# Kernel tuning notes

Hardware: AMD Instinct MI355X
Metric: run time of the kernel (lower is better)

Reference implementation:

```python
import jax, jax.numpy as jnp
import numpy as np

EPS = 1e-5  # BatchNorm eps


def setup_inputs() -> dict:
    key = jax.random.key(0)
    ks = jax.random.split(key, 13)
    B, C, H, W = 8, 256, 64, 64
    Ci = 128
    s = 0.05
    return {
        "x": jax.random.normal(ks[0], (B, C, H, W), jnp.float32),
        "Wt": jax.random.normal(ks[1], (Ci, C), jnp.float32) * s,
        "bt": jax.random.normal(ks[2], (Ci,), jnp.float32) * s,
        "Wp": jax.random.normal(ks[3], (Ci, C), jnp.float32) * s,
        "bp": jax.random.normal(ks[4], (Ci,), jnp.float32) * s,
        "Wg": jax.random.normal(ks[5], (Ci, C), jnp.float32) * s,
        "bg": jax.random.normal(ks[6], (Ci,), jnp.float32) * s,
        "Wz": jax.random.normal(ks[7], (C, Ci), jnp.float32) * s,
        "bz": jax.random.normal(ks[8], (C,), jnp.float32) * s,
        "gamma": jax.random.normal(ks[9], (C,), jnp.float32) * s,
        "beta": jax.random.normal(ks[10], (C,), jnp.float32) * s,
        "rmean": jax.random.normal(ks[11], (C,), jnp.float32) * s,
        "rvar": jax.random.uniform(ks[12], (C,), jnp.float32, 0.5, 1.5),
    }


def reference(x, Wt, bt, Wp, bp, Wg, bg, Wz, bz, gamma, beta, rmean, rvar):
    B, C, H, W = x.shape
    N = H * W
    xf = x.reshape(B, C, N)                                  # [B,C,N]
    # 1x1 conv projections == channel GEMMs
    theta = jnp.einsum('oc,bcn->bno', Wt, xf) + bt           # [B,N,Ci]
    phi = jnp.einsum('oc,bcn->bon', Wp, xf) + bp[:, None]    # [B,Ci,N]
    g = jnp.einsum('oc,bcn->bno', Wg, xf) + bg               # [B,N,Ci]
    # single-head attention over all N=H*W positions
    attn = jax.nn.softmax(jnp.einsum('bnc,bcm->bnm', theta, phi), axis=-1)
    y = jnp.einsum('bnm,bmc->bnc', attn, g)                  # [B,N,Ci]
    # W_z: 1x1 conv + BatchNorm (eval mode: running stats) + residual
    z = jnp.einsum('oc,bnc->bon', Wz, y) + bz[:, None]       # [B,C,N]
    inv = gamma / jnp.sqrt(rvar + EPS)                       # [C]
    zn = (z - rmean[:, None]) * inv[:, None] + beta[:, None]
    return zn.reshape(B, C, H, W) + x
```

## Files before the change

### kernel.cpp

```cpp
#include <hip/hip_runtime.h>
#include <stdint.h>

typedef __attribute__((ext_vector_type(8))) short bf16x8;
typedef __attribute__((ext_vector_type(4))) float f32x4;
typedef __attribute__((ext_vector_type(16))) float f32x16;

__device__ __forceinline__ unsigned short f32_to_bf16(float f) {
  union { float f; uint32_t u; } v; v.f = f;
  uint32_t u = v.u;
  u += 0x7fffu + ((u >> 16) & 1u);
  return (unsigned short)(u >> 16);
}

__device__ __forceinline__ float bf16_to_f32(unsigned short s) {
  union { uint32_t u; float f; } v; v.u = ((uint32_t)s) << 16;
  return v.f;
}

__device__ __forceinline__ uint32_t cvt_pk_bf16(float a, float b) {
  uint32_t r;
  asm("v_cvt_pk_bf16_f32 %0, %1, %2" : "=v"(r) : "v"(a), "v"(b));
  return r;
}

__device__ __forceinline__ void async_copy16(void* lds, const void* g) {
  __builtin_amdgcn_global_load_lds(
      (const __attribute__((address_space(1))) unsigned int*)g,
      (__attribute__((address_space(3))) unsigned int*)lds, 16, 0, 0);
}

__global__ __launch_bounds__(256) void wcvt_kernel(
    const float* __restrict__ Wt, const float* __restrict__ Wp,
    const float* __restrict__ Wg, const float* __restrict__ Wz,
    unsigned short* __restrict__ Wcat, unsigned short* __restrict__ Wzb) {
  int e = (blockIdx.x * 256 + threadIdx.x) * 4;
  const float* src;
  unsigned short* dst;
  int off;
  if (e < 32768) { src = Wt; dst = Wcat; off = e; }
  else if (e < 65536) { src = Wp; dst = Wcat + 32768; off = e - 32768; }
  else if (e < 98304) { src = Wg; dst = Wcat + 65536; off = e - 65536; }
  else { src = Wz; dst = Wzb; off = e - 98304; }
  float4 v = *(const float4*)(src + off);
  union { uint2 u; unsigned short s[4]; } pk;
  pk.s[0] = f32_to_bf16(v.x); pk.s[1] = f32_to_bf16(v.y);
  pk.s[2] = f32_to_bf16(v.z); pk.s[3] = f32_to_bf16(v.w);
  *(uint2*)(dst + off) = pk.u;
}

__global__ __launch_bounds__(512, 2) void proj_kernel(
    const float* __restrict__ x,
    const unsigned short* __restrict__ Wcat,
    const float* __restrict__ bt, const float* __restrict__ bp,
    const float* __restrict__ bg,
    unsigned short* __restrict__ Q, unsigned short* __restrict__ Km,
    unsigned short* __restrict__ Vt) {
  __shared__ __align__(1024) unsigned short xs[128 * 256];
  __shared__ unsigned short tmp[32][132];
  const int t = threadIdx.x;
  const int lane = t & 63;
  const int w = t >> 6;
  const int nt = blockIdx.x;
  const int b = blockIdx.y;
  const int n0 = nt * 128;

  const float* xb = x + (size_t)b * 256 * 4096;
  unsigned char* lbase = (unsigned char*)xs;

  for (int cc = 0; cc < 8; ++cc) {
#pragma unroll
    for (int i = 0; i < 2; ++i) {
      int idx = i * 512 + t;
      int c = idx >> 5;
      int n4 = (idx & 31) * 4;
      float4 v = *(const float4*)(xb + (size_t)(cc * 32 + c) * 4096 + n0 + n4);
      union { uint2 u; unsigned short s[4]; } pk;
      pk.s[0] = f32_to_bf16(v.x); pk.s[1] = f32_to_bf16(v.y);
      pk.s[2] = f32_to_bf16(v.z); pk.s[3] = f32_to_bf16(v.w);
      *(uint2*)&tmp[c][n4] = pk.u;
    }
    __syncthreads();
    {
      int n = t >> 2;
      int ch = t & 3;
      union { uint4 u; unsigned short s[8]; } pk;
#pragma unroll
      for (int jj = 0; jj < 8; ++jj) pk.s[jj] = tmp[ch * 8 + jj][n];
      int byt = n * 512 + ((cc * 64 + ch * 16) ^ ((n & 7) << 4));
      *(uint4*)(lbase + byt) = pk.u;
    }
    __syncthreads();
  }

  const int rl = lane & 15, gh = lane >> 4;
  const int swz = (rl & 7) << 4;
  const int rlv = (rl & 3) | ((rl & 4) << 1) | ((rl & 8) >> 1);

  f32x4 aQ[8], aK[8], aV[8];
#pragma unroll
  for (int i = 0; i < 8; ++i) {
    aQ[i] = (f32x4){0.f, 0.f, 0.f, 0.f};
    aK[i] = (f32x4){0.f, 0.f, 0.f, 0.f};
    aV[i] = (f32x4){0.f, 0.f, 0.f, 0.f};
  }

  const unsigned char* wq =
      (const unsigned char*)Wcat + ((w * 16 + rl) * 256) * 2 + gh * 16;
  const unsigned char* wk = wq + 128 * 512;
  const unsigned char* wv = wq + 256 * 512;

#pragma unroll
  for (int kk = 0; kk < 8; ++kk) {
    bf16x8 xf[8];
#pragma unroll
    for (int n2 = 0; n2 < 8; ++n2)
      xf[n2] = *(const bf16x8*)(lbase + (n2 * 16 + rl) * 512 +
                                ((kk * 64 + gh * 16) ^ swz));
    bf16x8 fq = *(const bf16x8*)(wq + kk * 64);
    bf16x8 fk = *(const bf16x8*)(wk + kk * 64);
    bf16x8 fv = *(const bf16x8*)(wv + kk * 64);
#pragma unroll
    for (int n2 = 0; n2 < 8; ++n2) {
      aQ[n2] = __builtin_amdgcn_mfma_f32_16x16x32_bf16(xf[n2], fq, aQ[n2], 0, 0, 0);
      aK[n2] = __builtin_amdgcn_mfma_f32_16x16x32_bf16(xf[n2], fk, aK[n2], 0, 0, 0);
      aV[n2] = __builtin_amdgcn_mfma_f32_16x16x32_bf16(fv, xf[n2], aV[n2], 0, 0, 0);
    }
  }

  const float btv = bt[w * 16 + rl];
  const float bpv = bp[w * 16 + rl];
  float bgv[4];
#pragma unroll
  for (int j = 0; j < 4; ++j) bgv[j] = bg[w * 16 + gh * 4 + j];

  unsigned short* Qb = Q + ((size_t)b * 4096 + n0) * 128 + w * 16 + rl;
  unsigned short* Kb = Km + ((size_t)b * 4096 + n0) * 128 + w * 16 + rl;
  unsigned short* Vb = Vt + (size_t)b * 128 * 4096 + n0 + rlv;
#pragma unroll
  for (int n2 = 0; n2 < 8; ++n2) {
#pragma unroll
    for (int j = 0; j < 4; ++j) {
      int n = n2 * 16 + gh * 4 + j;
      Qb[(size_t)n * 128] = f32_to_bf16(aQ[n2][j] + btv);
      Kb[(size_t)n * 128] = f32_to_bf16(aK[n2][j] + bpv);
      int o = w * 16 + gh * 4 + j;
      Vb[(size_t)o * 4096 + n2 * 16] = f32_to_bf16(aV[n2][j] + bgv[j]);
    }
  }
}

__global__ __launch_bounds__(256, 2) void attn_kernel(
    const unsigned short* __restrict__ Qg,
    const unsigned short* __restrict__ Kg,
    const unsigned short* __restrict__ Vg,
    unsigned short* __restrict__ Opart,
    float* __restrict__ Marr, float* __restrict__ Larr) {
  __shared__ __align__(1024) unsigned char smem[65536];
  const int t = threadIdx.x;
  const int lane = t & 63;
  const int w = t >> 6;
  const int q31 = lane & 31;
  const int hi = lane >> 5;
  const int kswz = (q31 & 15) << 4;

  const int orig = blockIdx.x;
  const int b = orig & 7;
  const int idx = orig >> 3;
  const int h = idx & 1;
  const int qg = idx >> 1;
  const int qw = qg * 128 + w * 32;
  const int kv0 = h * 2048;

  const unsigned short* Qb = Qg + (size_t)b * 4096 * 128;
  const unsigned short* Kb = Kg + (size_t)b * 4096 * 128;
  const unsigned short* Vb = Vg + (size_t)b * 128 * 4096;

  bf16x8 qf[8];
  {
    const unsigned char* qp =
        (const unsigned char*)(Qb + (size_t)(qw + q31) * 128) + hi * 16;
#pragma unroll
    for (int dc = 0; dc < 8; ++dc) qf[dc] = *(const bf16x8*)(qp + dc * 32);
  }

  const unsigned char* ksrc[4];
  const unsigned char* vsrc[4];
  unsigned int kofs[4], vofs[4];
#pragma unroll
  for (int ii = 0; ii < 4; ++ii) {
    int seg = w * 4 + ii;
    {
      int r = seg * 4 + (lane >> 4);
      int kcol = ((lane & 15) * 16) ^ ((r & 15) << 4);
      ksrc[ii] = (const unsigned char*)(Kb + (size_t)(kv0 + r) * 128) + kcol;
      kofs[ii] = seg * 1024;
    }
    {
      int o = seg * 1024 + lane * 16;
      int R = o >> 8;
      int cp = (o & 255) ^ ((R & 15) << 4);
      int d = 2 * R + (cp >> 7);
      int kvb = cp & 127;
      vsrc[ii] = (const unsigned char*)(Vb + (size_t)d * 4096 + kv0) + kvb;
      vofs[ii] = 16384 + seg * 1024;
    }
  }

  f32x16 acc[4];
#pragma unroll
  for (int i = 0; i < 4; ++i)
#pragma unroll
    for (int e = 0; e < 16; ++e) acc[i][e] = 0.f;
  float m = -1e30f, l = 0.f;

#pragma unroll
  for (int ii = 0; ii < 4; ++ii) {
    async_copy16(smem + kofs[ii], ksrc[ii]);
    async_copy16(smem + vofs[ii], vsrc[ii]);
  }
  __syncthreads();

#pragma unroll 2
  for (int it = 0; it < 32; ++it) {
    unsigned char* bb = smem + (it & 1) * 32768;
    if (it + 1 < 32) {
      unsigned int nb = ((it + 1) & 1) * 32768;
      size_t ko = (size_t)(it + 1) * 16384;
      int vo2 = (it + 1) * 128;
#pragma unroll
      for (int ii = 0; ii < 4; ++ii) {
        async_copy16(smem + nb + kofs[ii], ksrc[ii] + ko);
        async_copy16(smem + nb + vofs[ii], vsrc[ii] + vo2);
      }
    }

    f32x16 st0, st1;
#pragma unroll
    for (int e = 0; e < 16; ++e) { st0[e] = 0.f; st1[e] = 0.f; }
    const unsigned char* kb0 = bb + q31 * 256;
    const unsigned char* kb1 = bb + (32 + q31) * 256;
    __builtin_amdgcn_s_setprio(1);
#pragma unroll
    for (int dc = 0; dc < 8; ++dc) {
      int off = (dc * 32 + hi * 16) ^ kswz;
      bf16x8 k0 = *(const bf16x8*)(kb0 + off);
      bf16x8 k1 = *(const bf16x8*)(kb1 + off);
      st0 = __builtin_amdgcn_mfma_f32_32x32x16_bf16(k0, qf[dc], st0, 0, 0, 0);
      st1 = __builtin_amdgcn_mfma_f32_32x32x16_bf16(k1, qf[dc], st1, 0, 0, 0);
    }
    __builtin_amdgcn_s_setprio(0);

    float t8[8];
#pragma unroll
    for (int e = 0; e < 8; ++e)
      t8[e] = fmaxf(fmaxf(st0[e], st0[e + 8]), fmaxf(st1[e], st1[e + 8]));
#pragma unroll
    for (int e = 0; e < 4; ++e) t8[e] = fmaxf(t8[e], t8[e + 4]);
    float tl = fmaxf(fmaxf(t8[0], t8[1]), fmaxf(t8[2], t8[3]));
    if (__any(tl > m + 8.f)) {
      float tmax = tl;
#pragma unroll
      for (int off = 1; off < 64; off <<= 1)
        tmax = fmaxf(tmax, __shfl_xor(tmax, off));
      float mn = fmaxf(m, tmax);
      float sc = __expf(m - mn);
      m = mn;
      l *= sc;
#pragma unroll
      for (int i = 0; i < 4; ++i)
#pragma unroll
        for (int e = 0; e < 16; ++e) acc[i][e] *= sc;
    }
    float ls = 0.f;
#pragma unroll
    for (int e = 0; e < 16; ++e) { st0[e] = __expf(st0[e] - m); ls += st0[e]; }
#pragma unroll
    for (int e = 0; e < 16; ++e) { st1[e] = __expf(st1[e] - m); ls += st1[e]; }
    l += ls;

    const unsigned char* vbase = bb + 16384 + (q31 >> 1) * 256;
    const int vhb = (q31 & 1) << 7;
    const int vswz = (q31 >> 1) << 4;
#pragma unroll
    for (int ks = 0; ks < 4; ++ks) {
      union { uint32_t u[4]; bf16x8 v; } pk;
      if (ks == 0) {
        pk.u[0] = cvt_pk_bf16(st0[0], st0[1]);
        pk.u[1] = cvt_pk_bf16(st0[2], st0[3]);
        pk.u[2] = cvt_pk_bf16(st0[4], st0[5]);
        pk.u[3] = cvt_pk_bf16(st0[6], st0[7]);
      } else if (ks == 1) {
        pk.u[0] = cvt_pk_bf16(st0[8], st0[9]);
        pk.u[1] = cvt_pk_bf16(st0[10], st0[11]);
        pk.u[2] = cvt_pk_bf16(st0[12], st0[13]);
        pk.u[3] = cvt_pk_bf16(st0[14], st0[15]);
      } else if (ks == 2) {
        pk.u[0] = cvt_pk_bf16(st1[0], st1[1]);
        pk.u[1] = cvt_pk_bf16(st1[2], st1[3]);
        pk.u[2] = cvt_pk_bf16(st1[4], st1[5]);
        pk.u[3] = cvt_pk_bf16(st1[6], st1[7]);
      } else {
        pk.u[0] = cvt_pk_bf16(st1[8], st1[9]);
        pk.u[1] = cvt_pk_bf16(st1[10], st1[11]);
        pk.u[2] = cvt_pk_bf16(st1[12], st1[13]);
        pk.u[3] = cvt_pk_bf16(st1[14], st1[15]);
      }
      __builtin_amdgcn_s_setprio(1);
#pragma unroll
      for (int dt = 0; dt < 4; ++dt) {
        bf16x8 vf = *(const bf16x8*)(
            vbase + dt * 4096 + ((vhb | (ks * 32 + hi * 16)) ^ vswz));
        acc[dt] = __builtin_amdgcn_mfma_f32_32x32x16_bf16(pk.v, vf, acc[dt], 0, 0, 0);
      }
      __builtin_amdgcn_s_setprio(0);
    }
    __syncthreads();
  }

  float lf = l + __shfl_xor(l, 32);
  if (lane < 32) {
    size_t ix = (size_t)h * 32768 + (size_t)b * 4096 + qw + q31;
    Marr[ix] = m;
    Larr[ix] = lf;
  }
  unsigned short* ob = Opart + (size_t)h * 32768 * 128;
#pragma unroll
  for (int dt = 0; dt < 4; ++dt)
#pragma unroll
    for (int r = 0; r < 16; ++r) {
      int qrow = qw + (r & 3) + 8 * (r >> 2) + 4 * hi;
      ob[((size_t)b * 4096 + qrow) * 128 + dt * 32 + q31] =
          f32_to_bf16(acc[dt][r]);
    }
}

__global__ __launch_bounds__(512, 2) void outz_kernel(
    const unsigned short* __restrict__ Opart,
    const float* __restrict__ Marr, const float* __restrict__ Larr,
    const unsigned short* __restrict__ Wzb,
    const float* __restrict__ x, const float* __restrict__ bz,
    const float* __restrict__ gamma, const float* __restrict__ beta,
    const float* __restrict__ rmean, const float* __restrict__ rvar,
    float* __restrict__ out) {
  __shared__ __align__(1024) unsigned short ys[128 * 128];
  const int t = threadIdx.x;
  const int lane = t & 63;
  const int w = t >> 6;
  const int nt = blockIdx.x;
  const int b = blockIdx.y;
  const int n0 = nt * 128;

  unsigned char* lbase = (unsigned char*)ys;
#pragma unroll
  for (int i = 0; i < 4; ++i) {
    int off = (w * 4 + i) * 1024 + lane * 16;
    int n = off >> 8;
    int cb = (off & 255) ^ ((n & 7) << 4);
    size_t qidx = (size_t)b * 4096 + n0 + n;
    float m0 = Marr[qidx], m1 = Marr[32768 + qidx];
    float l0 = Larr[qidx], l1 = Larr[32768 + qidx];
    float M = fmaxf(m0, m1);
    float e0 = __expf(m0 - M), e1 = __expf(m1 - M);
    float rd = 1.f / (e0 * l0 + e1 * l1);
    float f0 = e0 * rd, f1 = e1 * rd;
    const unsigned char* ob = (const unsigned char*)Opart;
    const bf16x8 o0 = *(const bf16x8*)(ob + qidx * 256 + cb);
    const bf16x8 o1 = *(const bf16x8*)(ob + 32768ull * 256 + qidx * 256 + cb);
    union { uint4 u4; unsigned short s[8]; } pk;
#pragma unroll
    for (int e = 0; e < 8; ++e)
      pk.s[e] = f32_to_bf16(f0 * bf16_to_f32((unsigned short)o0[e]) +
                            f1 * bf16_to_f32((unsigned short)o1[e]));
    *(uint4*)(lbase + off) = pk.u4;
  }
  __syncthreads();

  const int rl = lane & 15, gh = lane >> 4;
  const int swz = (rl & 7) << 4;

  f32x4 acc[2][8];
#pragma unroll
  for (int i = 0; i < 2; ++i)
#pragma unroll
    for (int j = 0; j < 8; ++j) acc[i][j] = (f32x4){0.f, 0.f, 0.f, 0.f};

  const unsigned char* wz0 =
      (const unsigned char*)Wzb + ((w * 2) * 16 + rl) * 256 + gh * 16;

#pragma unroll
  for (int kk = 0; kk < 4; ++kk) {
    bf16x8 yf[8];
#pragma unroll
    for (int n2 = 0; n2 < 8; ++n2)
      yf[n2] = *(const bf16x8*)(lbase + (n2 * 16 + rl) * 256 +
                                ((kk * 64 + gh * 16) ^ swz));
    bf16x8 f0 = *(const bf16x8*)(wz0 + kk * 64);
    bf16x8 f1 = *(const bf16x8*)(wz0 + 16 * 256 + kk * 64);
#pragma unroll
    for (int n2 = 0; n2 < 8; ++n2) {
      acc[0][n2] = __builtin_amdgcn_mfma_f32_16x16x32_bf16(f0, yf[n2], acc[0][n2], 0, 0, 0);
      acc[1][n2] = __builtin_amdgcn_mfma_f32_16x16x32_bf16(f1, yf[n2], acc[1][n2], 0, 0, 0);
    }
  }

#pragma unroll
  for (int ot = 0; ot < 2; ++ot) {
#pragma unroll
    for (int j = 0; j < 4; ++j) {
      int o = (w * 2 + ot) * 16 + gh * 4 + j;
      float scale = gamma[o] * rsqrtf(rvar[o] + 1e-5f);
      float shift = (bz[o] - rmean[o]) * scale + beta[o];
      const float* xr = x + ((size_t)b * 256 + o) * 4096 + n0;
      float* orow = out + ((size_t)b * 256 + o) * 4096 + n0;
#pragma unroll
      for (int n2 = 0; n2 < 8; ++n2) {
        int n = n2 * 16 + rl;
        orow[n] = acc[ot][n2][j] * scale + shift + xr[n];
      }
    }
  }
}

extern "C" void kernel_launch(void* const* d_in, const int* in_sizes, int n_in,
                              void* d_out, int out_size, void* d_ws,
                              size_t ws_size, hipStream_t stream) {
  const float* x     = (const float*)d_in[0];
  const float* Wt    = (const float*)d_in[1];
  const float* bt    = (const float*)d_in[2];
  const float* Wp    = (const float*)d_in[3];
  const float* bp    = (const float*)d_in[4];
  const float* Wg    = (const float*)d_in[5];
  const float* bg    = (const float*)d_in[6];
  const float* Wz    = (const float*)d_in[7];
  const float* bz    = (const float*)d_in[8];
  const float* gamma = (const float*)d_in[9];
  const float* beta  = (const float*)d_in[10];
  const float* rmean = (const float*)d_in[11];
  const float* rvar  = (const float*)d_in[12];
  float* out = (float*)d_out;

  const size_t NE = (size_t)8 * 4096 * 128;
  unsigned short* Wcat  = (unsigned short*)d_ws;
  unsigned short* Wzb   = Wcat + 98304;
  float*          Marr  = (float*)(Wzb + 32768);
  float*          Larr  = Marr + 2 * 32768;
  unsigned short* Opart = (unsigned short*)(Larr + 2 * 32768);
  unsigned short* Q     = Opart + 2 * NE;
  unsigned short* Km    = Q + NE;
  unsigned short* Vt    = Km + NE;

  wcvt_kernel<<<128, 256, 0, stream>>>(Wt, Wp, Wg, Wz, Wcat, Wzb);
  proj_kernel<<<dim3(32, 8), 512, 0, stream>>>(x, Wcat, bt, bp, bg, Q, Km, Vt);
  attn_kernel<<<512, 256, 0, stream>>>(Q, Km, Vt, Opart, Marr, Larr);
  outz_kernel<<<dim3(32, 8), 512, 0, stream>>>(Opart, Marr, Larr, Wzb, x, bz,
                                               gamma, beta, rmean, rvar, out);
}
```

Baseline: 124.3 us.

## Process 64 query rows per wave in attention to reuse K/V fragments

Each attention wave now handles two 32-row query tiles that share every K and V fragment read from LDS. This halves LDS traffic per MFMA, and the block count drops from 512 to 256 since each block covers 256 queries. The cost is roughly double the accumulator and query registers, so launch bounds drop to one block per SM, unroll drops to 1, and only 256 blocks are launched, which leaves fewer waves to hide latency and may underfill the 256 CUs.

New measurement: 142.2 us. 14.4% more time.

```diff
diff --git a/kernel.cpp b/kernel.cpp
--- a/kernel.cpp
+++ b/kernel.cpp
@@ -149,7 +149,7 @@
   }
 }
 
-__global__ __launch_bounds__(256, 2) void attn_kernel(
+__global__ __launch_bounds__(256, 1) void attn_kernel(
     const unsigned short* __restrict__ Qg,
     const unsigned short* __restrict__ Kg,
     const unsigned short* __restrict__ Vg,
@@ -168,19 +168,23 @@
   const int idx = orig >> 3;
   const int h = idx & 1;
   const int qg = idx >> 1;
-  const int qw = qg * 128 + w * 32;
+  const int qw = qg * 256 + w * 64;
   const int kv0 = h * 2048;
 
   const unsigned short* Qb = Qg + (size_t)b * 4096 * 128;
   const unsigned short* Kb = Kg + (size_t)b * 4096 * 128;
   const unsigned short* Vb = Vg + (size_t)b * 128 * 4096;
 
-  bf16x8 qf[8];
+  bf16x8 qfA[8], qfB[8];
   {
-    const unsigned char* qp =
+    const unsigned char* qpA =
         (const unsigned char*)(Qb + (size_t)(qw + q31) * 128) + hi * 16;
-#pragma unroll
-    for (int dc = 0; dc < 8; ++dc) qf[dc] = *(const bf16x8*)(qp + dc * 32);
+    const unsigned char* qpB = qpA + 32 * 256;
+#pragma unroll
+    for (int dc = 0; dc < 8; ++dc) {
+      qfA[dc] = *(const bf16x8*)(qpA + dc * 32);
+      qfB[dc] = *(const bf16x8*)(qpB + dc * 32);
+    }
   }
 
   const unsigned char* ksrc[4];
@@ -206,12 +210,12 @@
     }
   }
 
-  f32x16 acc[4];
+  f32x16 accA[4], accB[4];
 #pragma unroll
   for (int i = 0; i < 4; ++i)
 #pragma unroll
-    for (int e = 0; e < 16; ++e) acc[i][e] = 0.f;
-  float m = -1e30f, l = 0.f;
+    for (int e = 0; e < 16; ++e) { accA[i][e] = 0.f; accB[i][e] = 0.f; }
+  float m = -1e30f, lA = 0.f, lB = 0.f;
 
 #pragma unroll
   for (int ii = 0; ii < 4; ++ii) {
@@ -220,7 +224,7 @@
   }
   __syncthreads();
 
-#pragma unroll 2
+#pragma unroll 1
   for (int it = 0; it < 32; ++it) {
     unsigned char* bb = smem + (it & 1) * 32768;
     if (it + 1 < 32) {
@@ -234,103 +238,97 @@
       }
     }
 
-    f32x16 st0, st1;
-#pragma unroll
-    for (int e = 0; e < 16; ++e) { st0[e] = 0.f; st1[e] = 0.f; }
-    const unsigned char* kb0 = bb + q31 * 256;
-    const unsigned char* kb1 = bb + (32 + q31) * 256;
-    __builtin_amdgcn_s_setprio(1);
-#pragma unroll
-    for (int dc = 0; dc < 8; ++dc) {
-      int off = (dc * 32 + hi * 16) ^ kswz;
-      bf16x8 k0 = *(const bf16x8*)(kb0 + off);
-      bf16x8 k1 = *(const bf16x8*)(kb1 + off);
-      st0 = __builtin_amdgcn_mfma_f32_32x32x16_bf16(k0, qf[dc], st0, 0, 0, 0);
-      st1 = __builtin_amdgcn_mfma_f32_32x32x16_bf16(k1, qf[dc], st1, 0, 0, 0);
-    }
-    __builtin_amdgcn_s_setprio(0);
-
-    float t8[8];
-#pragma unroll
-    for (int e = 0; e < 8; ++e)
-      t8[e] = fmaxf(fmaxf(st0[e], st0[e + 8]), fmaxf(st1[e], st1[e + 8]));
-#pragma unroll
-    for (int e = 0; e < 4; ++e) t8[e] = fmaxf(t8[e], t8[e + 4]);
-    float tl = fmaxf(fmaxf(t8[0], t8[1]), fmaxf(t8[2], t8[3]));
-    if (__any(tl > m + 8.f)) {
-      float tmax = tl;
-#pragma unroll
-      for (int off = 1; off < 64; off <<= 1)
-        tmax = fmaxf(tmax, __shfl_xor(tmax, off));
-      float mn = fmaxf(m, tmax);
-      float sc = __expf(m - mn);
-      m = mn;
-      l *= sc;
-#pragma unroll
-      for (int i = 0; i < 4; ++i)
-#pragma unroll
-        for (int e = 0; e < 16; ++e) acc[i][e] *= sc;
-    }
-    float ls = 0.f;
-#pragma unroll
-    for (int e = 0; e < 16; ++e) { st0[e] = __expf(st0[e] - m); ls += st0[e]; }
-#pragma unroll
-    for (int e = 0; e < 16; ++e) { st1[e] = __expf(st1[e] - m); ls += st1[e]; }
-    l += ls;
-
     const unsigned char* vbase = bb + 16384 + (q31 >> 1) * 256;
     const int vhb = (q31 & 1) << 7;
     const int vswz = (q31 >> 1) << 4;
-#pragma unroll
-    for (int ks = 0; ks < 4; ++ks) {
-      union { uint32_t u[4]; bf16x8 v; } pk;
-      if (ks == 0) {
-        pk.u[0] = cvt_pk_bf16(st0[0], st0[1]);
-        pk.u[1] = cvt_pk_bf16(st0[2], st0[3]);
-        pk.u[2] = cvt_pk_bf16(st0[4], st0[5]);
-        pk.u[3] = cvt_pk_bf16(st0[6], st0[7]);
-      } else if (ks == 1) {
-        pk.u[0] = cvt_pk_bf16(st0[8], st0[9]);
-        pk.u[1] = cvt_pk_bf16(st0[10], st0[11]);
-        pk.u[2] = cvt_pk_bf16(st0[12], st0[13]);
-        pk.u[3] = cvt_pk_bf16(st0[14], st0[15]);
-      } else if (ks == 2) {
-        pk.u[0] = cvt_pk_bf16(st1[0], st1[1]);
-        pk.u[1] = cvt_pk_bf16(st1[2], st1[3]);
-        pk.u[2] = cvt_pk_bf16(st1[4], st1[5]);
-        pk.u[3] = cvt_pk_bf16(st1[6], st1[7]);
-      } else {
-        pk.u[0] = cvt_pk_bf16(st1[8], st1[9]);
-        pk.u[1] = cvt_pk_bf16(st1[10], st1[11]);
-        pk.u[2] = cvt_pk_bf16(st1[12], st1[13]);
-        pk.u[3] = cvt_pk_bf16(st1[14], st1[15]);
-      }
+
+#pragma unroll
+    for (int tile = 0; tile < 2; ++tile) {
+      f32x16 sA, sB;
+#pragma unroll
+      for (int e = 0; e < 16; ++e) { sA[e] = 0.f; sB[e] = 0.f; }
+      const unsigned char* kb = bb + (tile * 32 + q31) * 256;
       __builtin_amdgcn_s_setprio(1);
 #pragma unroll
-      for (int dt = 0; dt < 4; ++dt) {
-        bf16x8 vf = *(const bf16x8*)(
-            vbase + dt * 4096 + ((vhb | (ks * 32 + hi * 16)) ^ vswz));
-        acc[dt] = __builtin_amdgcn_mfma_f32_32x32x16_bf16(pk.v, vf, acc[dt], 0, 0, 0);
+      for (int dc = 0; dc < 8; ++dc) {
+        bf16x8 kf = *(const bf16x8*)(kb + ((dc * 32 + hi * 16) ^ kswz));
+        sA = __builtin_amdgcn_mfma_f32_32x32x16_bf16(kf, qfA[dc], sA, 0, 0, 0);
+        sB = __builtin_amdgcn_mfma_f32_32x32x16_bf16(kf, qfB[dc], sB, 0, 0, 0);
       }
       __builtin_amdgcn_s_setprio(0);
+
+      float t8[8];
+#pragma unroll
+      for (int e = 0; e < 8; ++e)
+        t8[e] = fmaxf(fmaxf(sA[e], sA[e + 8]), fmaxf(sB[e], sB[e + 8]));
+#pragma unroll
+      for (int e = 0; e < 4; ++e) t8[e] = fmaxf(t8[e], t8[e + 4]);
+      float tl = fmaxf(fmaxf(t8[0], t8[1]), fmaxf(t8[2], t8[3]));
+      if (__any(tl > m + 8.f)) {
+        float tmax = tl;
+#pragma unroll
+        for (int off = 1; off < 64; off <<= 1)
+          tmax = fmaxf(tmax, __shfl_xor(tmax, off));
+        float mn = fmaxf(m, tmax);
+        float sc = __expf(m - mn);
+        m = mn;
+        lA *= sc; lB *= sc;
+#pragma unroll
+        for (int i = 0; i < 4; ++i)
+#pragma unroll
+          for (int e = 0; e < 16; ++e) { accA[i][e] *= sc; accB[i][e] *= sc; }
+      }
+      float a0 = 0.f, a1 = 0.f, b0 = 0.f, b1 = 0.f;
+#pragma unroll
+      for (int e = 0; e < 8; ++e) {
+        sA[e] = __expf(sA[e] - m);       a0 += sA[e];
+        sA[e + 8] = __expf(sA[e + 8] - m); a1 += sA[e + 8];
+        sB[e] = __expf(sB[e] - m);       b0 += sB[e];
+        sB[e + 8] = __expf(sB[e + 8] - m); b1 += sB[e + 8];
+      }
+      lA += a0 + a1;
+      lB += b0 + b1;
+
+#pragma unroll
+      for (int ksi = 0; ksi < 2; ++ksi) {
+        int ks = tile * 2 + ksi;
+        union { uint32_t u[4]; bf16x8 v; } pkA, pkB;
+#pragma unroll
+        for (int j = 0; j < 4; ++j) {
+          pkA.u[j] = cvt_pk_bf16(sA[ksi * 8 + j * 2], sA[ksi * 8 + j * 2 + 1]);
+          pkB.u[j] = cvt_pk_bf16(sB[ksi * 8 + j * 2], sB[ksi * 8 + j * 2 + 1]);
+        }
+        __builtin_amdgcn_s_setprio(1);
+#pragma unroll
+        for (int dt = 0; dt < 4; ++dt) {
+          bf16x8 vf = *(const bf16x8*)(
+              vbase + dt * 4096 + ((vhb | (ks * 32 + hi * 16)) ^ vswz));
+          accA[dt] = __builtin_amdgcn_mfma_f32_32x32x16_bf16(pkA.v, vf, accA[dt], 0, 0, 0);
+          accB[dt] = __builtin_amdgcn_mfma_f32_32x32x16_bf16(pkB.v, vf, accB[dt], 0, 0, 0);
+        }
+        __builtin_amdgcn_s_setprio(0);
+      }
     }
     __syncthreads();
   }
 
-  float lf = l + __shfl_xor(l, 32);
+  float lfA = lA + __shfl_xor(lA, 32);
+  float lfB = lB + __shfl_xor(lB, 32);
   if (lane < 32) {
     size_t ix = (size_t)h * 32768 + (size_t)b * 4096 + qw + q31;
-    Marr[ix] = m;
-    Larr[ix] = lf;
+    Marr[ix] = m;      Larr[ix] = lfA;
+    Marr[ix + 32] = m; Larr[ix + 32] = lfB;
   }
   unsigned short* ob = Opart + (size_t)h * 32768 * 128;
 #pragma unroll
   for (int dt = 0; dt < 4; ++dt)
 #pragma unroll
     for (int r = 0; r < 16; ++r) {
-      int qrow = qw + (r & 3) + 8 * (r >> 2) + 4 * hi;
-      ob[((size_t)b * 4096 + qrow) * 128 + dt * 32 + q31] =
-          f32_to_bf16(acc[dt][r]);
+      int crow = (r & 3) + 8 * (r >> 2) + 4 * hi;
+      ob[((size_t)b * 4096 + qw + crow) * 128 + dt * 32 + q31] =
+          f32_to_bf16(accA[dt][r]);
+      ob[((size_t)b * 4096 + qw + 32 + crow) * 128 + dt * 32 + q31] =
+          f32_to_bf16(accB[dt][r]);
     }
 }
 
@@ -451,7 +449,7 @@
 
   wcvt_kernel<<<128, 256, 0, stream>>>(Wt, Wp, Wg, Wz, Wcat, Wzb);
   proj_kernel<<<dim3(32, 8), 512, 0, stream>>>(x, Wcat, bt, bp, bg, Q, Km, Vt);
-  attn_kernel<<<512, 256, 0, stream>>>(Q, Km, Vt, Opart, Marr, Larr);
+  attn_kernel<<<256, 256, 0, stream>>>(Q, Km, Vt, Opart, Marr, Larr);
   outz_kernel<<<dim3(32, 8), 512, 0, stream>>>(Opart, Marr, Larr, Wzb, x, bz,
                                                gamma, beta, rmean, rvar, out);
 }
```
